# Optimization experiments

Measured on AMD Instinct MI355X. Metric: run time of the kernel, lower is better.

## Reference

```python
import jax, jax.numpy as jnp
import numpy as np

K, N, E, D = 4, 2048, 4096, 128
BETA = 0.6
EPS = 0.01           # epsilon in hard-sigmoid gating
LAM = 0.05           # lambda_schedule
TC0, TCMAX = 0.3, 0.7
COS_EPS = 1e-8       # F.cosine_similarity eps
MAX_SCORED_EDGES = 500
EDGE_DENSITY = 0.008


def setup_inputs() -> dict:
    key = jax.random.key(0)
    ks = jax.random.split(key, 8)
    s = 0.02
    H = (jax.random.uniform(ks[0], (K, N, E)) < EDGE_DENSITY).astype(jnp.float32)
    X = jax.random.normal(ks[1], (N, D), jnp.float32)
    return dict(
        H=H, X=X, epoch=50,
        mlp_w1=jax.random.normal(ks[2], (K, D, D), jnp.float32) * s,
        mlp_b1=jnp.zeros((K, D), jnp.float32),
        mlp_w2=jax.random.normal(ks[3], (K, D, D), jnp.float32) * s,
        mlp_b2=jnp.zeros((K, D), jnp.float32),
        comp_W=jax.random.normal(ks[4], (K, D, D), jnp.float32) * 0.01,
        att_w1=jax.random.normal(ks[5], (K, D, D // 2), jnp.float32) * s,
        att_b1=jnp.zeros((K, D // 2), jnp.float32),
        att_w2=jax.random.normal(ks[6], (K, D // 2, 1), jnp.float32) * s,
        att_b2=jnp.zeros((K, 1), jnp.float32),
    )


def reference(H, X, epoch, mlp_w1, mlp_b1, mlp_w2, mlp_b2, comp_W,
              att_w1, att_b1, att_w2, att_b2):
    # ---- component level (Eq. 4, batched over K) ----
    h1 = jax.nn.relu(jnp.einsum('nd,kdh->knh', X, mlp_w1) + mlp_b1[:, None, :])
    Xk = jnp.einsum('knh,khe->kne', h1, mlp_w2) + mlp_b2[:, None, :]        # [K,N,D]
    a1 = jax.nn.relu(jnp.einsum('knd,kdh->knh', Xk, att_w1) + att_b1[:, None, :])
    att = jax.nn.sigmoid(jnp.einsum('knh,kho->kno', a1, att_w2) + att_b2[:, None, :])
    S_att = att.mean(axis=(1, 2))                                            # [K]
    frob = jnp.sqrt((comp_W ** 2).sum(axis=(1, 2)))                          # ||W_k||_F
    featn = jnp.sqrt((Xk ** 2).sum(axis=(1, 2)))                             # ||MLP(X_k)||_2 (Frobenius)
    imp = BETA * frob * featn + (1.0 - BETA) * S_att
    pi_c = jax.nn.softmax(imp)
    theta_c = TC0 + (1.0 - jnp.exp(-LAM * epoch)) * (TCMAX - TC0)            # Eq. 3 schedule
    gates = jnp.clip((pi_c - theta_c) / EPS + 0.5, 0.0, 1.0)                 # hard sigmoid
    # K_min = max(1, int(0.1*K)) = 1 -> force top-1 gate open
    keep = jax.nn.one_hot(jnp.argmax(gates), K, dtype=gates.dtype)
    gates = jnp.maximum(gates, keep)

    xnorm = jnp.linalg.norm(X, axis=1)                                       # [N]
    xhat = X / jnp.maximum(xnorm, COS_EPS)[:, None]
    er = jnp.arange(E)
    eye = jnp.eye(N, dtype=bool)

    Hp_l, eg_l, npi_l = [], [], []
    for k in range(K):  # small fixed component count
        Hk = H[k]
        mask = Hk > 0                                                        # [N,E]
        cnt = mask.sum(axis=0)                                               # nodes per hyperedge
        order = jnp.cumsum(mask, axis=0)
        i = jnp.argmax(mask, axis=0)                                         # first incident node
        j = jnp.argmax(mask & (order == 2), axis=0)                          # second incident node
        cos = (xhat[i] * xhat[j]).sum(-1)                                    # [E]
        A = Hk[i, er] * Hk[j, er]                                            # A_ij per edge
        # torch loop: only first 500 edges scored; <2-node edges get 0.1; rest 0
        imp_e = jnp.where(er < MAX_SCORED_EDGES,
                          jnp.where(cnt >= 2, A * cos, 0.1), 0.0)
        pi_e = jax.nn.softmax(imp_e)
        theta_e = jnp.minimum(theta_c, pi_e.mean() + jnp.std(pi_e, ddof=1))  # torch.std unbiased
        eg = jnp.clip((pi_e - theta_e) / EPS + 0.5, 0.0, 1.0)
        eg = jnp.where((eg.sum() < 1.0) & (er == jnp.argmax(pi_e)), 1.0, eg)
        eg_eff = jnp.where(gates[k] > 0.5, eg, jnp.ones_like(eg))
        Hp = Hk * gates[k] * eg_eff[None, :]                                 # pruned incidence

        # ---- node level (Eq. 7) on pruned graph ----
        B = (Hp > 0).astype(Hk.dtype)
        Adj = ((B @ B.T) > 0) & (~eye)                                       # shared-hyperedge neighbors
        degf = Adj.sum(axis=1).astype(Hk.dtype)
        nsum = Adj.astype(Hk.dtype) @ xhat                                   # sum of neighbor unit vecs
        avg = jnp.where(degf > 0, (xhat * nsum).sum(-1) / jnp.maximum(degf, 1.0), 0.0)
        npi = jax.nn.softmax(avg * xnorm)
        Hp_l.append(Hp); eg_l.append(eg); npi_l.append(npi)

    return (jnp.stack(Hp_l), gates, jnp.stack(eg_l), jnp.stack(npi_l))
```

## Files before the change

### kernel.cpp

```cpp
#include <hip/hip_runtime.h>
#include <math.h>

#define KCOMP 4
#define NN 2048
#define EE 4096
#define DD 128
#define MAXNE 96
#define MAXSE 500
#define BETA_C 0.6f
#define EPS_G 0.01f
#define LAM_S 0.05f
#define TC0_C 0.3f
#define TCMAX_C 0.7f
#define COS_EPS_C 1e-8f

static const size_t OFF_XHAT   = 0;
static const size_t OFF_XNORM  = 1048576;
static const size_t OFF_SCAL   = 1056768;
static const size_t OFF_NCNT   = 1057024;
static const size_t OFF_EMASK  = 1089792;
static const size_t OFF_NELIST = 5284096;
static const size_t OFF_IMPE   = 6856960;
static const size_t OFF_EGS    = 6865152;
static const size_t OFF_Z      = 6930688;

__global__ __launch_bounds__(1024) void k_scanx(
    const float4* __restrict__ H4, unsigned* __restrict__ emask,
    const float* __restrict__ X, float* __restrict__ xhat, float* __restrict__ xnorm,
    float* __restrict__ scal) {
  int b = blockIdx.x, t = threadIdx.x;
  if (b < 256) {
    __shared__ unsigned lds[256 * 17];
    int k = b >> 6;
    int rem = b & 63;
    int ch_super = rem >> 4;
    int e4_super = rem & 15;
    int chi = t >> 6;
    int e4i = t & 63;
    int ch = ch_super * 16 + chi;
    int e4 = e4_super * 64 + e4i;
    int n0 = ch * 32;
    const float4* p = H4 + ((size_t)(k * NN + n0)) * (EE / 4) + e4;
    unsigned w0 = 0, w1 = 0, w2 = 0, w3 = 0;
    for (int rb = 0; rb < 32; rb += 8) {
      float4 v[8];
#pragma unroll
      for (int u = 0; u < 8; ++u) v[u] = p[(size_t)(rb + u) * (EE / 4)];
#pragma unroll
      for (int u = 0; u < 8; ++u) {
        unsigned bit = 1u << (rb + u);
        w0 |= (v[u].x > 0.f) ? bit : 0u;
        w1 |= (v[u].y > 0.f) ? bit : 0u;
        w2 |= (v[u].z > 0.f) ? bit : 0u;
        w3 |= (v[u].w > 0.f) ? bit : 0u;
      }
    }
    int el = e4i * 4;
    lds[(el + 0) * 17 + chi] = w0;
    lds[(el + 1) * 17 + chi] = w1;
    lds[(el + 2) * 17 + chi] = w2;
    lds[(el + 3) * 17 + chi] = w3;
    __syncthreads();
    int e_base = e4_super * 256;
    int wi = t & 15;
    int eo = t >> 4;
#pragma unroll
    for (int it = 0; it < 4; ++it) {
      int e_local = it * 64 + eo;
      emask[((size_t)(k * EE) + e_base + e_local) * 64 + ch_super * 16 + wi] =
          lds[e_local * 17 + wi];
    }
  } else {
    if (b == 256 && t < 64) scal[t] = 0.f;
    int node = (b - 256) * 16 + (t >> 6);
    int lane = t & 63;
    float2 v = ((const float2*)X)[(size_t)node * 64 + lane];
    float ss = v.x * v.x + v.y * v.y;
    for (int o = 32; o > 0; o >>= 1) ss += __shfl_xor(ss, o, 64);
    float nrm = sqrtf(ss);
    float den = fmaxf(nrm, COS_EPS_C);
    if (lane == 0) xnorm[node] = nrm;
    float2 o2; o2.x = v.x / den; o2.y = v.y / den;
    ((float2*)xhat)[(size_t)node * 64 + lane] = o2;
  }
}

__global__ void k_mlnel(const float* __restrict__ X,
                        const float* __restrict__ w1, const float* __restrict__ b1,
                        const float* __restrict__ w2, const float* __restrict__ b2,
                        const float* __restrict__ aw1, const float* __restrict__ ab1,
                        const float* __restrict__ aw2, const float* __restrict__ ab2,
                        const float4* __restrict__ compW4, float* __restrict__ scal,
                        const unsigned* __restrict__ emask, int* __restrict__ ncnt,
                        unsigned short* __restrict__ nelist, const float* __restrict__ xhat,
                        float* __restrict__ impE) {
  __shared__ char smem[28736];
  int t = threadIdx.x;
  int k = blockIdx.y;
  int bx = blockIdx.x;
  if (bx >= 208) {
    int e = (bx - 208) * 4 + (t >> 6);
    int lane = t & 63;
    unsigned w = emask[((size_t)(k * EE) + e) * 64 + lane];
    int pc = __popc(w);
    for (int o = 32; o > 0; o >>= 1) pc += __shfl_xor(pc, o, 64);
    float impv = 0.1f;
    if (pc >= 2) {
      unsigned l1 = w ? (unsigned)((lane << 5) + __builtin_ctz(w)) : 0xffffffffu;
      unsigned wr = w & (w - 1);
      unsigned l2 = wr ? (unsigned)((lane << 5) + __builtin_ctz(wr)) : 0xffffffffu;
      unsigned g1 = l1;
      for (int o = 32; o > 0; o >>= 1) {
        unsigned x = (unsigned)__shfl_xor((int)g1, o, 64);
        g1 = g1 < x ? g1 : x;
      }
      unsigned cand = (l1 == g1) ? l2 : l1;
      unsigned g2 = cand;
      for (int o = 32; o > 0; o >>= 1) {
        unsigned x = (unsigned)__shfl_xor((int)g2, o, 64);
        g2 = g2 < x ? g2 : x;
      }
      float2 xi = ((const float2*)xhat)[(size_t)g1 * 64 + lane];
      float2 xj = ((const float2*)xhat)[(size_t)g2 * 64 + lane];
      float d = xi.x * xj.x + xi.y * xj.y;
      for (int o = 32; o > 0; o >>= 1) d += __shfl_xor(d, o, 64);
      impv = d;
    }
    if (lane == 0) impE[k * 512 + e] = impv;
    return;
  }
  if (bx >= 144) {
    unsigned short* lst = (unsigned short*)smem;
    int* lcnt = (int*)(smem + 32 * MAXNE * 2);
    int w = bx - 144;
    if (t < 32) lcnt[t] = 0;
    __syncthreads();
    for (int e = t; e < EE; e += 256) {
      unsigned wd = emask[((size_t)(k * EE) + e) * 64 + w];
      while (wd) {
        int b = __builtin_ctz(wd); wd &= wd - 1;
        int slot = atomicAdd(&lcnt[b], 1);
        if (slot < MAXNE) lst[b * MAXNE + slot] = (unsigned short)e;
      }
    }
    __syncthreads();
    if (t < 32) ncnt[k * NN + w * 32 + t] = lcnt[t];
    for (int i = t; i < 32 * MAXNE; i += 256) {
      int b = i / MAXNE, s = i - b * MAXNE;
      int c = lcnt[b]; if (c > MAXNE) c = MAXNE;
      if (s < c) nelist[((size_t)(k * NN + w * 32 + b)) * MAXNE + s] = lst[b * MAXNE + s];
    }
    return;
  }
  float* Xs  = (float*)smem;
  float* H1s = Xs + 2048;
  float* XKs = H1s + 2048;
  float* A1s = XKs + 2048;
  float* red = A1s + 1024;
  if (bx >= 128) {
    float4 v = compW4[(size_t)k * 4096 + (bx - 128) * 256 + t];
    float s = v.x * v.x + v.y * v.y + v.z * v.z + v.w * v.w;
    for (int o = 32; o > 0; o >>= 1) s += __shfl_xor(s, o, 64);
    if ((t & 63) == 0) red[t >> 6] = s;
    __syncthreads();
    if (t == 0) atomicAdd(&scal[8 + k], red[0] + red[1] + red[2] + red[3]);
    return;
  }
  int n0 = bx * 16;
  for (int i = t; i < 16 * 128; i += 256) Xs[i] = X[(size_t)n0 * 128 + i];
  __syncthreads();

  int h = t & 127, g = t >> 7;
  const float* W1 = w1 + (size_t)k * 128 * 128;
  float acc[8];
  float bb = b1[k * 128 + h];
#pragma unroll
  for (int i = 0; i < 8; i++) acc[i] = bb;
  for (int d = 0; d < 128; ++d) {
    float w = W1[d * 128 + h];
#pragma unroll
    for (int i = 0; i < 8; i++) acc[i] = fmaf(Xs[(g * 8 + i) * 128 + d], w, acc[i]);
  }
#pragma unroll
  for (int i = 0; i < 8; i++) H1s[(g * 8 + i) * 128 + h] = fmaxf(acc[i], 0.f);
  __syncthreads();

  const float* W2 = w2 + (size_t)k * 128 * 128;
  bb = b2[k * 128 + h];
#pragma unroll
  for (int i = 0; i < 8; i++) acc[i] = bb;
  for (int d = 0; d < 128; ++d) {
    float w = W2[d * 128 + h];
#pragma unroll
    for (int i = 0; i < 8; i++) acc[i] = fmaf(H1s[(g * 8 + i) * 128 + d], w, acc[i]);
  }
  float fpart = 0.f;
#pragma unroll
  for (int i = 0; i < 8; i++) { XKs[(g * 8 + i) * 128 + h] = acc[i]; fpart = fmaf(acc[i], acc[i], fpart); }
  __syncthreads();

  int h2 = t & 63, g4 = t >> 6;
  const float* AW1 = aw1 + (size_t)k * 128 * 64;
  float a4[4];
  float ab = ab1[k * 64 + h2];
#pragma unroll
  for (int i = 0; i < 4; i++) a4[i] = ab;
  for (int d = 0; d < 128; ++d) {
    float w = AW1[d * 64 + h2];
#pragma unroll
    for (int i = 0; i < 4; i++) a4[i] = fmaf(XKs[(g4 * 4 + i) * 128 + d], w, a4[i]);
  }
#pragma unroll
  for (int i = 0; i < 4; i++) A1s[(g4 * 4 + i) * 64 + h2] = fmaxf(a4[i], 0.f);
  __syncthreads();

  float attsum = 0.f;
  if (t < 16) {
    const float* AW2 = aw2 + (size_t)k * 64;
    float a = ab2[k];
    for (int d = 0; d < 64; ++d) a = fmaf(A1s[t * 64 + d], AW2[d], a);
    attsum = 1.f / (1.f + expf(-a));
  }
  for (int o = 32; o > 0; o >>= 1) {
    fpart  += __shfl_xor(fpart, o, 64);
    attsum += __shfl_xor(attsum, o, 64);
  }
  int wv = t >> 6, ln = t & 63;
  if (ln == 0) { red[wv] = fpart; red[8 + wv] = attsum; }
  __syncthreads();
  if (t == 0) {
    float fs = red[0] + red[1] + red[2] + red[3];
    float as = red[8] + red[9] + red[10] + red[11];
    atomicAdd(&scal[0 + k], fs);
    atomicAdd(&scal[4 + k], as);
  }
}

__device__ __forceinline__ float blockReduceSum16(float v, float* red, int t) {
  for (int o = 32; o > 0; o >>= 1) v += __shfl_xor(v, o, 64);
  __syncthreads();
  if ((t & 63) == 0) red[t >> 6] = v;
  __syncthreads();
  float s = red[0];
#pragma unroll
  for (int i = 1; i < 16; i++) s += red[i];
  return s;
}

__global__ void k_edgegate(const float* __restrict__ impE, float* __restrict__ scal,
                           const int* __restrict__ epoch, float* __restrict__ out_gates,
                           float* __restrict__ egscaled, float* __restrict__ out_eg) {
  __shared__ float red[16];
  __shared__ int redi[16];
  int k = blockIdx.x;
  int t = threadIdx.x;
  float gates[KCOMP];
  float tc;
  {
    float imp[KCOMP];
    for (int kk = 0; kk < KCOMP; kk++) {
      float featn = sqrtf(scal[0 + kk]);
      float satt  = scal[4 + kk] / (float)NN;
      float frob  = sqrtf(scal[8 + kk]);
      imp[kk] = BETA_C * frob * featn + (1.f - BETA_C) * satt;
    }
    float mx = imp[0];
    for (int kk = 1; kk < KCOMP; kk++) mx = fmaxf(mx, imp[kk]);
    float ex[KCOMP], ssum = 0.f;
    for (int kk = 0; kk < KCOMP; kk++) { ex[kk] = expf(imp[kk] - mx); ssum += ex[kk]; }
    tc = TC0_C + (1.f - expf(-LAM_S * (float)epoch[0])) * (TCMAX_C - TC0_C);
    for (int kk = 0; kk < KCOMP; kk++) {
      float pi = ex[kk] / ssum;
      gates[kk] = fminf(fmaxf((pi - tc) / EPS_G + 0.5f, 0.f), 1.f);
    }
    int am = 0; float bv2 = gates[0];
    for (int kk = 1; kk < KCOMP; kk++) if (gates[kk] > bv2) { bv2 = gates[kk]; am = kk; }
    gates[am] = fmaxf(gates[am], 1.f);
  }
  if (t == 0) {
    scal[12 + k] = gates[k];
    if (k == 0) for (int kk = 0; kk < KCOMP; kk++) out_gates[kk] = gates[kk];
  }
  float imp[4];
#pragma unroll
  for (int j = 0; j < 4; j++) {
    int e = t + j * 1024;
    imp[j] = (e < MAXSE) ? impE[k * 512 + e] : 0.f;
  }
  float m = fmaxf(fmaxf(imp[0], imp[1]), fmaxf(imp[2], imp[3]));
  for (int o = 32; o > 0; o >>= 1) m = fmaxf(m, __shfl_xor(m, o, 64));
  __syncthreads();
  if ((t & 63) == 0) red[t >> 6] = m;
  __syncthreads();
  m = red[0];
#pragma unroll
  for (int i = 1; i < 16; i++) m = fmaxf(m, red[i]);
  float p[4], psum = 0.f;
#pragma unroll
  for (int j = 0; j < 4; j++) { p[j] = expf(imp[j] - m); psum += p[j]; }
  float S = blockReduceSum16(psum, red, t);
  float pi[4], tot = 0.f;
#pragma unroll
  for (int j = 0; j < 4; j++) { pi[j] = p[j] / S; tot += pi[j]; }
  float T = blockReduceSum16(tot, red, t);
  float mean = T / (float)EE;
  float devs = 0.f;
#pragma unroll
  for (int j = 0; j < 4; j++) { float d = pi[j] - mean; devs = fmaf(d, d, devs); }
  float V = blockReduceSum16(devs, red, t);
  float stdv = sqrtf(V / (float)(EE - 1));
  float theta = fminf(tc, mean + stdv);
  float eg[4], egsum = 0.f;
#pragma unroll
  for (int j = 0; j < 4; j++) {
    eg[j] = fminf(fmaxf((pi[j] - theta) / EPS_G + 0.5f, 0.f), 1.f);
    egsum += eg[j];
  }
  float EGS = blockReduceSum16(egsum, red, t);
  float bv = -1e30f; int bi = 0x7fffffff;
#pragma unroll
  for (int j = 0; j < 4; j++) if (pi[j] > bv) { bv = pi[j]; bi = t + j * 1024; }
  for (int o = 32; o > 0; o >>= 1) {
    float ov = __shfl_xor(bv, o, 64); int oi = __shfl_xor(bi, o, 64);
    if (ov > bv || (ov == bv && oi < bi)) { bv = ov; bi = oi; }
  }
  __syncthreads();
  if ((t & 63) == 0) { red[t >> 6] = bv; redi[t >> 6] = bi; }
  __syncthreads();
  float abv = red[0]; int abi = redi[0];
#pragma unroll
  for (int i = 1; i < 16; i++) {
    float ov = red[i]; int oi = redi[i];
    if (ov > abv || (ov == abv && oi < abi)) { abv = ov; abi = oi; }
  }
  float g = gates[k];
#pragma unroll
  for (int j = 0; j < 4; j++) {
    int e = t + j * 1024;
    float egv = eg[j];
    if (EGS < 1.f && e == abi) egv = 1.f;
    out_eg[(size_t)k * EE + e] = egv;
    float eff = (g > 0.5f) ? egv : 1.f;
    egscaled[k * EE + e] = g * eff;
  }
}

__global__ void k_hprow(const unsigned* __restrict__ emask,
                        const int* __restrict__ ncnt, const unsigned short* __restrict__ nelist,
                        const float* __restrict__ egs, const float* __restrict__ scal,
                        const float* __restrict__ xhat, const float* __restrict__ xnorm,
                        float* __restrict__ out, float* __restrict__ z) {
  __shared__ float row[EE];
  __shared__ unsigned short elds[MAXNE];
  __shared__ unsigned wpart[4][64];
  __shared__ unsigned short list[2048];
  __shared__ int cnt_s;
  __shared__ float sred[4];
  int k = blockIdx.y, n = blockIdx.x, t = threadIdx.x;
  float g = scal[12 + k];
  float4* o4 = (float4*)(out + ((size_t)(k * NN + n)) * EE);
  if (g <= 0.f) {
    float4 z4 = {0.f, 0.f, 0.f, 0.f};
#pragma unroll
    for (int i = 0; i < 4; i++) o4[t + i * 256] = z4;
    if (t == 0) z[k * NN + n] = 0.f;
    return;
  }
  int ec = ncnt[k * NN + n]; if (ec > MAXNE) ec = MAXNE;
  if (t < ec) elds[t] = nelist[((size_t)(k * NN + n)) * MAXNE + t];
  float4* row4 = (float4*)row;
  float4 z4 = {0.f, 0.f, 0.f, 0.f};
#pragma unroll
  for (int i = 0; i < 4; i++) row4[t + i * 256] = z4;
  if (t == 0) cnt_s = 0;
  __syncthreads();
  if (t < ec) {
    int e = elds[t];
    row[e] = egs[k * EE + e];
  }
  __syncthreads();
#pragma unroll
  for (int i = 0; i < 4; i++) o4[t + i * 256] = row4[t + i * 256];
  int lane = t & 63, wv = t >> 6;
  unsigned acc = 0;
  for (int it = wv; it < ec; it += 4) {
    int e = (int)elds[it];
    if (row[e] > 0.f) acc |= emask[((size_t)(k * EE) + e) * 64 + lane];
  }
  wpart[wv][lane] = acc;
  __syncthreads();
  if (t < 64) {
    unsigned w = wpart[0][t] | wpart[1][t] | wpart[2][t] | wpart[3][t];
    if (t == (n >> 5)) w &= ~(1u << (n & 31));
    int c = __popc(w);
    if (c > 0) {
      int base = atomicAdd(&cnt_s, c);
      while (w) {
        int b = __builtin_ctz(w); w &= w - 1;
        list[base++] = (unsigned short)((t << 5) + b);
      }
    }
  }
  __syncthreads();
  int cnt = cnt_s;
  if (cnt == 0) { if (t == 0) z[k * NN + n] = 0.f; return; }
  int fc = lane & 31, hh = lane >> 5;
  float4 xn4 = ((const float4*)xhat)[(size_t)n * 32 + fc];
  float a = 0.f;
  for (int it = wv * 2 + hh; it < cnt; it += 8) {
    int m = (int)list[it];
    float4 xm = ((const float4*)xhat)[(size_t)m * 32 + fc];
    a += xn4.x * xm.x + xn4.y * xm.y + xn4.z * xm.z + xn4.w * xm.w;
  }
  for (int o = 32; o > 0; o >>= 1) a += __shfl_xor(a, o, 64);
  if (lane == 0) sred[wv] = a;
  __syncthreads();
  if (t == 0) {
    float s = sred[0] + sred[1] + sred[2] + sred[3];
    z[k * NN + n] = (s / (float)cnt) * xnorm[n];
  }
}

__global__ void k_npi(const float* __restrict__ z, float* __restrict__ out_npi) {
  __shared__ float red[4];
  int k = blockIdx.x, t = threadIdx.x;
  float v[8]; float m = -1e30f;
#pragma unroll
  for (int j = 0; j < 8; j++) { v[j] = z[k * NN + t + j * 256]; m = fmaxf(m, v[j]); }
  for (int o = 32; o > 0; o >>= 1) m = fmaxf(m, __shfl_xor(m, o, 64));
  if ((t & 63) == 0) red[t >> 6] = m;
  __syncthreads();
  m = fmaxf(fmaxf(red[0], red[1]), fmaxf(red[2], red[3]));
  __syncthreads();
  float pe[8]; float s = 0.f;
#pragma unroll
  for (int j = 0; j < 8; j++) { pe[j] = expf(v[j] - m); s += pe[j]; }
  for (int o = 32; o > 0; o >>= 1) s += __shfl_xor(s, o, 64);
  if ((t & 63) == 0) red[t >> 6] = s;
  __syncthreads();
  s = red[0] + red[1] + red[2] + red[3];
#pragma unroll
  for (int j = 0; j < 8; j++) out_npi[k * NN + t + j * 256] = pe[j] / s;
}

extern "C" void kernel_launch(void* const* d_in, const int* in_sizes, int n_in,
                              void* d_out, int out_size, void* d_ws, size_t ws_size,
                              hipStream_t stream) {
  const float* H     = (const float*)d_in[0];
  const float* X     = (const float*)d_in[1];
  const int*   epoch = (const int*)d_in[2];
  const float* w1    = (const float*)d_in[3];
  const float* b1    = (const float*)d_in[4];
  const float* w2    = (const float*)d_in[5];
  const float* b2    = (const float*)d_in[6];
  const float* compW = (const float*)d_in[7];
  const float* aw1   = (const float*)d_in[8];
  const float* ab1   = (const float*)d_in[9];
  const float* aw2   = (const float*)d_in[10];
  const float* ab2   = (const float*)d_in[11];

  char* ws = (char*)d_ws;
  float* xhat  = (float*)(ws + OFF_XHAT);
  float* xnorm = (float*)(ws + OFF_XNORM);
  float* scal  = (float*)(ws + OFF_SCAL);
  int*   ncnt  = (int*)(ws + OFF_NCNT);
  unsigned* emask = (unsigned*)(ws + OFF_EMASK);
  unsigned short* nelist = (unsigned short*)(ws + OFF_NELIST);
  float* impE  = (float*)(ws + OFF_IMPE);
  float* egs   = (float*)(ws + OFF_EGS);
  float* zbuf  = (float*)(ws + OFF_Z);

  float* out       = (float*)d_out;
  float* out_gates = out + (size_t)KCOMP * NN * EE;
  float* out_eg    = out_gates + KCOMP;
  float* out_npi   = out_eg + (size_t)KCOMP * EE;

  k_scanx<<<384, 1024, 0, stream>>>((const float4*)H, emask, X, xhat, xnorm, scal);
  k_mlnel<<<dim3(333, KCOMP), 256, 0, stream>>>(X, w1, b1, w2, b2, aw1, ab1, aw2, ab2,
                                                (const float4*)compW, scal,
                                                emask, ncnt, nelist, xhat, impE);
  k_edgegate<<<KCOMP, 1024, 0, stream>>>(impE, scal, epoch, out_gates, egs, out_eg);
  k_hprow<<<dim3(NN, KCOMP), 256, 0, stream>>>(emask, ncnt, nelist, egs, scal, xhat, xnorm,
                                               out, zbuf);
  k_npi<<<KCOMP, 256, 0, stream>>>(zbuf, out_npi);
}
```

Baseline: 352.5 us.

## Fuse five kernels into three using last-block-done reductions

```diff
diff --git a/kernel.cpp b/kernel.cpp
--- a/kernel.cpp
+++ b/kernel.cpp
@@ -23,14 +23,24 @@
 static const size_t OFF_IMPE   = 6856960;
 static const size_t OFF_EGS    = 6865152;
 static const size_t OFF_Z      = 6930688;
-
-__global__ __launch_bounds__(1024) void k_scanx(
+static const size_t OFF_FEAT   = 6963456;
+static const size_t OFF_ATT    = 6965504;
+static const size_t OFF_FROB   = 6967552;
+
+__global__ __launch_bounds__(1024) void k_d1(
     const float4* __restrict__ H4, unsigned* __restrict__ emask,
     const float* __restrict__ X, float* __restrict__ xhat, float* __restrict__ xnorm,
-    float* __restrict__ scal) {
+    float* __restrict__ scal,
+    const float* __restrict__ w1, const float* __restrict__ b1,
+    const float* __restrict__ w2, const float* __restrict__ b2,
+    const float* __restrict__ aw1, const float* __restrict__ ab1,
+    const float* __restrict__ aw2, const float* __restrict__ ab2,
+    const float4* __restrict__ compW4,
+    float* __restrict__ featA, float* __restrict__ attA, float* __restrict__ frobA) {
+  __shared__ char smem[28928];
   int b = blockIdx.x, t = threadIdx.x;
   if (b < 256) {
-    __shared__ unsigned lds[256 * 17];
+    unsigned* lds = (unsigned*)smem;
     int k = b >> 6;
     int rem = b & 63;
     int ch_super = rem >> 4;
@@ -41,7 +51,7 @@
     int e4 = e4_super * 64 + e4i;
     int n0 = ch * 32;
     const float4* p = H4 + ((size_t)(k * NN + n0)) * (EE / 4) + e4;
-    unsigned w0 = 0, w1 = 0, w2 = 0, w3 = 0;
+    unsigned w0 = 0, w1b = 0, w2b = 0, w3 = 0;
     for (int rb = 0; rb < 32; rb += 8) {
       float4 v[8];
 #pragma unroll
@@ -49,16 +59,16 @@
 #pragma unroll
       for (int u = 0; u < 8; ++u) {
         unsigned bit = 1u << (rb + u);
-        w0 |= (v[u].x > 0.f) ? bit : 0u;
-        w1 |= (v[u].y > 0.f) ? bit : 0u;
-        w2 |= (v[u].z > 0.f) ? bit : 0u;
-        w3 |= (v[u].w > 0.f) ? bit : 0u;
+        w0  |= (v[u].x > 0.f) ? bit : 0u;
+        w1b |= (v[u].y > 0.f) ? bit : 0u;
+        w2b |= (v[u].z > 0.f) ? bit : 0u;
+        w3  |= (v[u].w > 0.f) ? bit : 0u;
       }
     }
     int el = e4i * 4;
     lds[(el + 0) * 17 + chi] = w0;
-    lds[(el + 1) * 17 + chi] = w1;
-    lds[(el + 2) * 17 + chi] = w2;
+    lds[(el + 1) * 17 + chi] = w1b;
+    lds[(el + 2) * 17 + chi] = w2b;
     lds[(el + 3) * 17 + chi] = w3;
     __syncthreads();
     int e_base = e4_super * 256;
@@ -70,7 +80,9 @@
       emask[((size_t)(k * EE) + e_base + e_local) * 64 + ch_super * 16 + wi] =
           lds[e_local * 17 + wi];
     }
-  } else {
+    return;
+  }
+  if (b < 384) {
     if (b == 256 && t < 64) scal[t] = 0.f;
     int node = (b - 256) * 16 + (t >> 6);
     int lane = t & 63;
@@ -82,24 +94,138 @@
     if (lane == 0) xnorm[node] = nrm;
     float2 o2; o2.x = v.x / den; o2.y = v.y / den;
     ((float2*)xhat)[(size_t)node * 64 + lane] = o2;
+    return;
+  }
+  if (b < 896) {
+    int mb = b - 384;
+    int k = mb >> 7;
+    int bx = mb & 127;
+    float* Xs  = (float*)smem;
+    float* H1s = Xs + 2048;
+    float* XKs = H1s + 2048;
+    float* A1s = XKs + 2048;
+    float* red = A1s + 1024;
+    int n0 = bx * 16;
+    for (int i = t; i < 16 * 128; i += 1024) Xs[i] = X[(size_t)n0 * 128 + i];
+    __syncthreads();
+
+    int h = t & 127, g = t >> 7;
+    const float* W1 = w1 + (size_t)k * 128 * 128;
+    float acc0 = b1[k * 128 + h], acc1 = acc0;
+    for (int d = 0; d < 128; ++d) {
+      float w = W1[d * 128 + h];
+      acc0 = fmaf(Xs[(g * 2 + 0) * 128 + d], w, acc0);
+      acc1 = fmaf(Xs[(g * 2 + 1) * 128 + d], w, acc1);
+    }
+    H1s[(g * 2 + 0) * 128 + h] = fmaxf(acc0, 0.f);
+    H1s[(g * 2 + 1) * 128 + h] = fmaxf(acc1, 0.f);
+    __syncthreads();
+
+    const float* W2 = w2 + (size_t)k * 128 * 128;
+    acc0 = b2[k * 128 + h]; acc1 = acc0;
+    for (int d = 0; d < 128; ++d) {
+      float w = W2[d * 128 + h];
+      acc0 = fmaf(H1s[(g * 2 + 0) * 128 + d], w, acc0);
+      acc1 = fmaf(H1s[(g * 2 + 1) * 128 + d], w, acc1);
+    }
+    float fpart = fmaf(acc1, acc1, acc0 * acc0);
+    XKs[(g * 2 + 0) * 128 + h] = acc0;
+    XKs[(g * 2 + 1) * 128 + h] = acc1;
+    __syncthreads();
+
+    int h2 = t & 63, g4 = t >> 6;
+    const float* AW1 = aw1 + (size_t)k * 128 * 64;
+    float a0 = ab1[k * 64 + h2];
+    for (int d = 0; d < 128; ++d) a0 = fmaf(XKs[g4 * 128 + d], AW1[d * 64 + h2], a0);
+    A1s[g4 * 64 + h2] = fmaxf(a0, 0.f);
+    __syncthreads();
+
+    float attsum = 0.f;
+    if (t < 16) {
+      const float* AW2 = aw2 + (size_t)k * 64;
+      float a = ab2[k];
+      for (int d = 0; d < 64; ++d) a = fmaf(A1s[t * 64 + d], AW2[d], a);
+      attsum = 1.f / (1.f + expf(-a));
+    }
+    for (int o = 32; o > 0; o >>= 1) {
+      fpart  += __shfl_xor(fpart, o, 64);
+      attsum += __shfl_xor(attsum, o, 64);
+    }
+    int wv = t >> 6, ln = t & 63;
+    if (ln == 0) { red[wv] = fpart; red[16 + wv] = attsum; }
+    __syncthreads();
+    if (t == 0) {
+      float fs = 0.f, as = 0.f;
+#pragma unroll
+      for (int i = 0; i < 16; i++) { fs += red[i]; as += red[16 + i]; }
+      featA[k * 128 + bx] = fs;
+      attA[k * 128 + bx]  = as;
+    }
+    return;
+  }
+  {
+    int fb = b - 896;
+    int k = fb >> 2, idx = fb & 3;
+    float* red = (float*)smem;
+    float4 v = compW4[(size_t)k * 4096 + idx * 1024 + t];
+    float s = v.x * v.x + v.y * v.y + v.z * v.z + v.w * v.w;
+    for (int o = 32; o > 0; o >>= 1) s += __shfl_xor(s, o, 64);
+    int wv = t >> 6, ln = t & 63;
+    if (ln == 0) red[wv] = s;
+    __syncthreads();
+    if (t == 0) {
+      float fs = 0.f;
+#pragma unroll
+      for (int i = 0; i < 16; i++) fs += red[i];
+      frobA[k * 4 + idx] = fs;
+    }
   }
 }
 
-__global__ void k_mlnel(const float* __restrict__ X,
-                        const float* __restrict__ w1, const float* __restrict__ b1,
-                        const float* __restrict__ w2, const float* __restrict__ b2,
-                        const float* __restrict__ aw1, const float* __restrict__ ab1,
-                        const float* __restrict__ aw2, const float* __restrict__ ab2,
-                        const float4* __restrict__ compW4, float* __restrict__ scal,
-                        const unsigned* __restrict__ emask, int* __restrict__ ncnt,
-                        unsigned short* __restrict__ nelist, const float* __restrict__ xhat,
-                        float* __restrict__ impE) {
-  __shared__ char smem[28736];
+__device__ __forceinline__ float bsum256(float v, volatile float* red, int t) {
+  for (int o = 32; o > 0; o >>= 1) v += __shfl_xor(v, o, 64);
+  __syncthreads();
+  if ((t & 63) == 0) red[t >> 6] = v;
+  __syncthreads();
+  return red[0] + red[1] + red[2] + red[3];
+}
+
+__global__ void k_d2(const unsigned* __restrict__ emask, int* __restrict__ ncnt,
+                     unsigned short* __restrict__ nelist, const float* __restrict__ xhat,
+                     float* __restrict__ impE, float* __restrict__ scal,
+                     const float* __restrict__ featA, const float* __restrict__ attA,
+                     const float* __restrict__ frobA, const int* __restrict__ epoch,
+                     float* __restrict__ out_gates, float* __restrict__ egs,
+                     float* __restrict__ out_eg) {
+  __shared__ char smem[32 * MAXNE * 2 + 128];
   int t = threadIdx.x;
   int k = blockIdx.y;
   int bx = blockIdx.x;
-  if (bx >= 208) {
-    int e = (bx - 208) * 4 + (t >> 6);
+  if (bx < 64) {
+    unsigned short* lst = (unsigned short*)smem;
+    int* lcnt = (int*)(smem + 32 * MAXNE * 2);
+    int w = bx;
+    if (t < 32) lcnt[t] = 0;
+    __syncthreads();
+    for (int e = t; e < EE; e += 256) {
+      unsigned wd = emask[((size_t)(k * EE) + e) * 64 + w];
+      while (wd) {
+        int b2 = __builtin_ctz(wd); wd &= wd - 1;
+        int slot = atomicAdd(&lcnt[b2], 1);
+        if (slot < MAXNE) lst[b2 * MAXNE + slot] = (unsigned short)e;
+      }
+    }
+    __syncthreads();
+    if (t < 32) ncnt[k * NN + w * 32 + t] = lcnt[t];
+    for (int i = t; i < 32 * MAXNE; i += 256) {
+      int b2 = i / MAXNE, s = i - b2 * MAXNE;
+      int c = lcnt[b2]; if (c > MAXNE) c = MAXNE;
+      if (s < c) nelist[((size_t)(k * NN + w * 32 + b2)) * MAXNE + s] = lst[b2 * MAXNE + s];
+    }
+    return;
+  }
+  {
+    int e = (bx - 64) * 4 + (t >> 6);
     int lane = t & 63;
     unsigned w = emask[((size_t)(k * EE) + e) * 64 + lane];
     int pc = __popc(w);
@@ -127,147 +253,41 @@
       impv = d;
     }
     if (lane == 0) impE[k * 512 + e] = impv;
-    return;
-  }
-  if (bx >= 144) {
-    unsigned short* lst = (unsigned short*)smem;
-    int* lcnt = (int*)(smem + 32 * MAXNE * 2);
-    int w = bx - 144;
-    if (t < 32) lcnt[t] = 0;
-    __syncthreads();
-    for (int e = t; e < EE; e += 256) {
-      unsigned wd = emask[((size_t)(k * EE) + e) * 64 + w];
-      while (wd) {
-        int b = __builtin_ctz(wd); wd &= wd - 1;
-        int slot = atomicAdd(&lcnt[b], 1);
-        if (slot < MAXNE) lst[b * MAXNE + slot] = (unsigned short)e;
-      }
-    }
-    __syncthreads();
-    if (t < 32) ncnt[k * NN + w * 32 + t] = lcnt[t];
-    for (int i = t; i < 32 * MAXNE; i += 256) {
-      int b = i / MAXNE, s = i - b * MAXNE;
-      int c = lcnt[b]; if (c > MAXNE) c = MAXNE;
-      if (s < c) nelist[((size_t)(k * NN + w * 32 + b)) * MAXNE + s] = lst[b * MAXNE + s];
-    }
-    return;
-  }
-  float* Xs  = (float*)smem;
-  float* H1s = Xs + 2048;
-  float* XKs = H1s + 2048;
-  float* A1s = XKs + 2048;
-  float* red = A1s + 1024;
-  if (bx >= 128) {
-    float4 v = compW4[(size_t)k * 4096 + (bx - 128) * 256 + t];
-    float s = v.x * v.x + v.y * v.y + v.z * v.z + v.w * v.w;
-    for (int o = 32; o > 0; o >>= 1) s += __shfl_xor(s, o, 64);
-    if ((t & 63) == 0) red[t >> 6] = s;
-    __syncthreads();
-    if (t == 0) atomicAdd(&scal[8 + k], red[0] + red[1] + red[2] + red[3]);
-    return;
-  }
-  int n0 = bx * 16;
-  for (int i = t; i < 16 * 128; i += 256) Xs[i] = X[(size_t)n0 * 128 + i];
-  __syncthreads();
-
-  int h = t & 127, g = t >> 7;
-  const float* W1 = w1 + (size_t)k * 128 * 128;
-  float acc[8];
-  float bb = b1[k * 128 + h];
-#pragma unroll
-  for (int i = 0; i < 8; i++) acc[i] = bb;
-  for (int d = 0; d < 128; ++d) {
-    float w = W1[d * 128 + h];
-#pragma unroll
-    for (int i = 0; i < 8; i++) acc[i] = fmaf(Xs[(g * 8 + i) * 128 + d], w, acc[i]);
-  }
-#pragma unroll
-  for (int i = 0; i < 8; i++) H1s[(g * 8 + i) * 128 + h] = fmaxf(acc[i], 0.f);
-  __syncthreads();
-
-  const float* W2 = w2 + (size_t)k * 128 * 128;
-  bb = b2[k * 128 + h];
-#pragma unroll
-  for (int i = 0; i < 8; i++) acc[i] = bb;
-  for (int d = 0; d < 128; ++d) {
-    float w = W2[d * 128 + h];
-#pragma unroll
-    for (int i = 0; i < 8; i++) acc[i] = fmaf(H1s[(g * 8 + i) * 128 + d], w, acc[i]);
-  }
-  float fpart = 0.f;
-#pragma unroll
-  for (int i = 0; i < 8; i++) { XKs[(g * 8 + i) * 128 + h] = acc[i]; fpart = fmaf(acc[i], acc[i], fpart); }
-  __syncthreads();
-
-  int h2 = t & 63, g4 = t >> 6;
-  const float* AW1 = aw1 + (size_t)k * 128 * 64;
-  float a4[4];
-  float ab = ab1[k * 64 + h2];
-#pragma unroll
-  for (int i = 0; i < 4; i++) a4[i] = ab;
-  for (int d = 0; d < 128; ++d) {
-    float w = AW1[d * 64 + h2];
-#pragma unroll
-    for (int i = 0; i < 4; i++) a4[i] = fmaf(XKs[(g4 * 4 + i) * 128 + d], w, a4[i]);
-  }
-#pragma unroll
-  for (int i = 0; i < 4; i++) A1s[(g4 * 4 + i) * 64 + h2] = fmaxf(a4[i], 0.f);
-  __syncthreads();
-
-  float attsum = 0.f;
-  if (t < 16) {
-    const float* AW2 = aw2 + (size_t)k * 64;
-    float a = ab2[k];
-    for (int d = 0; d < 64; ++d) a = fmaf(A1s[t * 64 + d], AW2[d], a);
-    attsum = 1.f / (1.f + expf(-a));
-  }
-  for (int o = 32; o > 0; o >>= 1) {
-    fpart  += __shfl_xor(fpart, o, 64);
-    attsum += __shfl_xor(attsum, o, 64);
-  }
+  }
+  __threadfence();
+  __shared__ int lastf;
+  if (t == 0) {
+    int old = atomicAdd((int*)scal + 16 + k, 1);
+    lastf = (old == 124);
+  }
+  __syncthreads();
+  if (!lastf) return;
+  __threadfence();
+
   int wv = t >> 6, ln = t & 63;
-  if (ln == 0) { red[wv] = fpart; red[8 + wv] = attsum; }
-  __syncthreads();
-  if (t == 0) {
-    float fs = red[0] + red[1] + red[2] + red[3];
-    float as = red[8] + red[9] + red[10] + red[11];
-    atomicAdd(&scal[0 + k], fs);
-    atomicAdd(&scal[4 + k], as);
-  }
-}
-
-__device__ __forceinline__ float blockReduceSum16(float v, float* red, int t) {
-  for (int o = 32; o > 0; o >>= 1) v += __shfl_xor(v, o, 64);
-  __syncthreads();
-  if ((t & 63) == 0) red[t >> 6] = v;
-  __syncthreads();
-  float s = red[0];
-#pragma unroll
-  for (int i = 1; i < 16; i++) s += red[i];
-  return s;
-}
-
-__global__ void k_edgegate(const float* __restrict__ impE, float* __restrict__ scal,
-                           const int* __restrict__ epoch, float* __restrict__ out_gates,
-                           float* __restrict__ egscaled, float* __restrict__ out_eg) {
-  __shared__ float red[16];
-  __shared__ int redi[16];
-  int k = blockIdx.x;
-  int t = threadIdx.x;
+  __shared__ float imps[KCOMP];
+  __shared__ float redf[4];
+  __shared__ int   redi[4];
+  {
+    float pf = 0.f, pa = 0.f;
+    for (int i = ln; i < 128; i += 64) { pf += featA[wv * 128 + i]; pa += attA[wv * 128 + i]; }
+    float pr = (ln < 4) ? frobA[wv * 4 + ln] : 0.f;
+    for (int o = 32; o > 0; o >>= 1) {
+      pf += __shfl_xor(pf, o, 64);
+      pa += __shfl_xor(pa, o, 64);
+      pr += __shfl_xor(pr, o, 64);
+    }
+    if (ln == 0)
+      imps[wv] = BETA_C * sqrtf(pr) * sqrtf(pf) + (1.f - BETA_C) * (pa / (float)NN);
+  }
+  __syncthreads();
   float gates[KCOMP];
   float tc;
   {
-    float imp[KCOMP];
-    for (int kk = 0; kk < KCOMP; kk++) {
-      float featn = sqrtf(scal[0 + kk]);
-      float satt  = scal[4 + kk] / (float)NN;
-      float frob  = sqrtf(scal[8 + kk]);
-      imp[kk] = BETA_C * frob * featn + (1.f - BETA_C) * satt;
-    }
-    float mx = imp[0];
-    for (int kk = 1; kk < KCOMP; kk++) mx = fmaxf(mx, imp[kk]);
+    float mx = imps[0];
+    for (int kk = 1; kk < KCOMP; kk++) mx = fmaxf(mx, imps[kk]);
     float ex[KCOMP], ssum = 0.f;
-    for (int kk = 0; kk < KCOMP; kk++) { ex[kk] = expf(imp[kk] - mx); ssum += ex[kk]; }
+    for (int kk = 0; kk < KCOMP; kk++) { ex[kk] = expf(imps[kk] - mx); ssum += ex[kk]; }
     tc = TC0_C + (1.f - expf(-LAM_S * (float)epoch[0])) * (TCMAX_C - TC0_C);
     for (int kk = 0; kk < KCOMP; kk++) {
       float pi = ex[kk] / ssum;
@@ -281,81 +301,88 @@
     scal[12 + k] = gates[k];
     if (k == 0) for (int kk = 0; kk < KCOMP; kk++) out_gates[kk] = gates[kk];
   }
-  float imp[4];
-#pragma unroll
-  for (int j = 0; j < 4; j++) {
-    int e = t + j * 1024;
-    imp[j] = (e < MAXSE) ? impE[k * 512 + e] : 0.f;
-  }
-  float m = fmaxf(fmaxf(imp[0], imp[1]), fmaxf(imp[2], imp[3]));
+
+  float ipj[16];
+#pragma unroll
+  for (int j = 0; j < 16; j++) {
+    int e = t + j * 256;
+    ipj[j] = (e < MAXSE) ? impE[k * 512 + e] : 0.f;
+  }
+  float m = ipj[0];
+#pragma unroll
+  for (int j = 1; j < 16; j++) m = fmaxf(m, ipj[j]);
   for (int o = 32; o > 0; o >>= 1) m = fmaxf(m, __shfl_xor(m, o, 64));
   __syncthreads();
-  if ((t & 63) == 0) red[t >> 6] = m;
-  __syncthreads();
-  m = red[0];
-#pragma unroll
-  for (int i = 1; i < 16; i++) m = fmaxf(m, red[i]);
-  float p[4], psum = 0.f;
-#pragma unroll
-  for (int j = 0; j < 4; j++) { p[j] = expf(imp[j] - m); psum += p[j]; }
-  float S = blockReduceSum16(psum, red, t);
-  float pi[4], tot = 0.f;
-#pragma unroll
-  for (int j = 0; j < 4; j++) { pi[j] = p[j] / S; tot += pi[j]; }
-  float T = blockReduceSum16(tot, red, t);
+  if (ln == 0) redf[wv] = m;
+  __syncthreads();
+  m = fmaxf(fmaxf(redf[0], redf[1]), fmaxf(redf[2], redf[3]));
+  float psum = 0.f;
+#pragma unroll
+  for (int j = 0; j < 16; j++) { ipj[j] = expf(ipj[j] - m); psum += ipj[j]; }
+  float S = bsum256(psum, redf, t);
+  float tot = 0.f;
+#pragma unroll
+  for (int j = 0; j < 16; j++) tot += ipj[j] / S;
+  float T = bsum256(tot, redf, t);
   float mean = T / (float)EE;
   float devs = 0.f;
 #pragma unroll
-  for (int j = 0; j < 4; j++) { float d = pi[j] - mean; devs = fmaf(d, d, devs); }
-  float V = blockReduceSum16(devs, red, t);
+  for (int j = 0; j < 16; j++) { float d = ipj[j] / S - mean; devs = fmaf(d, d, devs); }
+  float V = bsum256(devs, redf, t);
   float stdv = sqrtf(V / (float)(EE - 1));
   float theta = fminf(tc, mean + stdv);
-  float eg[4], egsum = 0.f;
-#pragma unroll
-  for (int j = 0; j < 4; j++) {
-    eg[j] = fminf(fmaxf((pi[j] - theta) / EPS_G + 0.5f, 0.f), 1.f);
-    egsum += eg[j];
-  }
-  float EGS = blockReduceSum16(egsum, red, t);
+  float egv[16];
+  float egsum = 0.f;
+#pragma unroll
+  for (int j = 0; j < 16; j++) {
+    egv[j] = fminf(fmaxf((ipj[j] / S - theta) / EPS_G + 0.5f, 0.f), 1.f);
+    egsum += egv[j];
+  }
+  float EGS = bsum256(egsum, redf, t);
   float bv = -1e30f; int bi = 0x7fffffff;
 #pragma unroll
-  for (int j = 0; j < 4; j++) if (pi[j] > bv) { bv = pi[j]; bi = t + j * 1024; }
+  for (int j = 0; j < 16; j++) {
+    float pi = ipj[j] / S;
+    if (pi > bv) { bv = pi; bi = t + j * 256; }
+  }
   for (int o = 32; o > 0; o >>= 1) {
     float ov = __shfl_xor(bv, o, 64); int oi = __shfl_xor(bi, o, 64);
     if (ov > bv || (ov == bv && oi < bi)) { bv = ov; bi = oi; }
   }
   __syncthreads();
-  if ((t & 63) == 0) { red[t >> 6] = bv; redi[t >> 6] = bi; }
-  __syncthreads();
-  float abv = red[0]; int abi = redi[0];
-#pragma unroll
-  for (int i = 1; i < 16; i++) {
-    float ov = red[i]; int oi = redi[i];
+  if (ln == 0) { redf[wv] = bv; redi[wv] = bi; }
+  __syncthreads();
+  float abv = redf[0]; int abi = redi[0];
+#pragma unroll
+  for (int i = 1; i < 4; i++) {
+    float ov = redf[i]; int oi = redi[i];
     if (ov > abv || (ov == abv && oi < abi)) { abv = ov; abi = oi; }
   }
   float g = gates[k];
 #pragma unroll
-  for (int j = 0; j < 4; j++) {
-    int e = t + j * 1024;
-    float egv = eg[j];
-    if (EGS < 1.f && e == abi) egv = 1.f;
-    out_eg[(size_t)k * EE + e] = egv;
-    float eff = (g > 0.5f) ? egv : 1.f;
-    egscaled[k * EE + e] = g * eff;
+  for (int j = 0; j < 16; j++) {
+    int e = t + j * 256;
+    float v = egv[j];
+    if (EGS < 1.f && e == abi) v = 1.f;
+    out_eg[(size_t)k * EE + e] = v;
+    float eff = (g > 0.5f) ? v : 1.f;
+    egs[k * EE + e] = g * eff;
   }
 }
 
 __global__ void k_hprow(const unsigned* __restrict__ emask,
                         const int* __restrict__ ncnt, const unsigned short* __restrict__ nelist,
-                        const float* __restrict__ egs, const float* __restrict__ scal,
+                        const float* __restrict__ egs, float* __restrict__ scal,
                         const float* __restrict__ xhat, const float* __restrict__ xnorm,
-                        float* __restrict__ out, float* __restrict__ z) {
+                        float* __restrict__ out, float* __restrict__ z,
+                        float* __restrict__ out_npi) {
   __shared__ float row[EE];
   __shared__ unsigned short elds[MAXNE];
   __shared__ unsigned wpart[4][64];
   __shared__ unsigned short list[2048];
   __shared__ int cnt_s;
   __shared__ float sred[4];
+  __shared__ int lastf;
   int k = blockIdx.y, n = blockIdx.x, t = threadIdx.x;
   float g = scal[12 + k];
   float4* o4 = (float4*)(out + ((size_t)(k * NN + n)) * EE);
@@ -364,83 +391,88 @@
 #pragma unroll
     for (int i = 0; i < 4; i++) o4[t + i * 256] = z4;
     if (t == 0) z[k * NN + n] = 0.f;
-    return;
-  }
-  int ec = ncnt[k * NN + n]; if (ec > MAXNE) ec = MAXNE;
-  if (t < ec) elds[t] = nelist[((size_t)(k * NN + n)) * MAXNE + t];
-  float4* row4 = (float4*)row;
-  float4 z4 = {0.f, 0.f, 0.f, 0.f};
-#pragma unroll
-  for (int i = 0; i < 4; i++) row4[t + i * 256] = z4;
-  if (t == 0) cnt_s = 0;
-  __syncthreads();
-  if (t < ec) {
-    int e = elds[t];
-    row[e] = egs[k * EE + e];
-  }
-  __syncthreads();
-#pragma unroll
-  for (int i = 0; i < 4; i++) o4[t + i * 256] = row4[t + i * 256];
-  int lane = t & 63, wv = t >> 6;
-  unsigned acc = 0;
-  for (int it = wv; it < ec; it += 4) {
-    int e = (int)elds[it];
-    if (row[e] > 0.f) acc |= emask[((size_t)(k * EE) + e) * 64 + lane];
-  }
-  wpart[wv][lane] = acc;
-  __syncthreads();
-  if (t < 64) {
-    unsigned w = wpart[0][t] | wpart[1][t] | wpart[2][t] | wpart[3][t];
-    if (t == (n >> 5)) w &= ~(1u << (n & 31));
-    int c = __popc(w);
-    if (c > 0) {
-      int base = atomicAdd(&cnt_s, c);
-      while (w) {
-        int b = __builtin_ctz(w); w &= w - 1;
-        list[base++] = (unsigned short)((t << 5) + b);
-      }
-    }
-  }
-  __syncthreads();
-  int cnt = cnt_s;
-  if (cnt == 0) { if (t == 0) z[k * NN + n] = 0.f; return; }
-  int fc = lane & 31, hh = lane >> 5;
-  float4 xn4 = ((const float4*)xhat)[(size_t)n * 32 + fc];
-  float a = 0.f;
-  for (int it = wv * 2 + hh; it < cnt; it += 8) {
-    int m = (int)list[it];
-    float4 xm = ((const float4*)xhat)[(size_t)m * 32 + fc];
-    a += xn4.x * xm.x + xn4.y * xm.y + xn4.z * xm.z + xn4.w * xm.w;
-  }
-  for (int o = 32; o > 0; o >>= 1) a += __shfl_xor(a, o, 64);
-  if (lane == 0) sred[wv] = a;
-  __syncthreads();
-  if (t == 0) {
-    float s = sred[0] + sred[1] + sred[2] + sred[3];
-    z[k * NN + n] = (s / (float)cnt) * xnorm[n];
-  }
-}
-
-__global__ void k_npi(const float* __restrict__ z, float* __restrict__ out_npi) {
-  __shared__ float red[4];
-  int k = blockIdx.x, t = threadIdx.x;
-  float v[8]; float m = -1e30f;
-#pragma unroll
-  for (int j = 0; j < 8; j++) { v[j] = z[k * NN + t + j * 256]; m = fmaxf(m, v[j]); }
-  for (int o = 32; o > 0; o >>= 1) m = fmaxf(m, __shfl_xor(m, o, 64));
-  if ((t & 63) == 0) red[t >> 6] = m;
-  __syncthreads();
-  m = fmaxf(fmaxf(red[0], red[1]), fmaxf(red[2], red[3]));
-  __syncthreads();
-  float pe[8]; float s = 0.f;
-#pragma unroll
-  for (int j = 0; j < 8; j++) { pe[j] = expf(v[j] - m); s += pe[j]; }
-  for (int o = 32; o > 0; o >>= 1) s += __shfl_xor(s, o, 64);
-  if ((t & 63) == 0) red[t >> 6] = s;
-  __syncthreads();
-  s = red[0] + red[1] + red[2] + red[3];
-#pragma unroll
-  for (int j = 0; j < 8; j++) out_npi[k * NN + t + j * 256] = pe[j] / s;
+  } else {
+    int ec = ncnt[k * NN + n]; if (ec > MAXNE) ec = MAXNE;
+    if (t < ec) elds[t] = nelist[((size_t)(k * NN + n)) * MAXNE + t];
+    float4* row4 = (float4*)row;
+    float4 z4 = {0.f, 0.f, 0.f, 0.f};
+#pragma unroll
+    for (int i = 0; i < 4; i++) row4[t + i * 256] = z4;
+    if (t == 0) cnt_s = 0;
+    __syncthreads();
+    if (t < ec) {
+      int e = elds[t];
+      row[e] = egs[k * EE + e];
+    }
+    __syncthreads();
+#pragma unroll
+    for (int i = 0; i < 4; i++) o4[t + i * 256] = row4[t + i * 256];
+    int lane = t & 63, wv = t >> 6;
+    unsigned acc = 0;
+    for (int it = wv; it < ec; it += 4) {
+      int e = (int)elds[it];
+      if (row[e] > 0.f) acc |= emask[((size_t)(k * EE) + e) * 64 + lane];
+    }
+    wpart[wv][lane] = acc;
+    __syncthreads();
+    if (t < 64) {
+      unsigned w = wpart[0][t] | wpart[1][t] | wpart[2][t] | wpart[3][t];
+      if (t == (n >> 5)) w &= ~(1u << (n & 31));
+      int c = __popc(w);
+      if (c > 0) {
+        int base = atomicAdd(&cnt_s, c);
+        while (w) {
+          int b = __builtin_ctz(w); w &= w - 1;
+          list[base++] = (unsigned short)((t << 5) + b);
+        }
+      }
+    }
+    __syncthreads();
+    int cnt = cnt_s;
+    if (cnt == 0) {
+      if (t == 0) z[k * NN + n] = 0.f;
+    } else {
+      int fc = lane & 31, hh = lane >> 5;
+      float4 xn4 = ((const float4*)xhat)[(size_t)n * 32 + fc];
+      float a = 0.f;
+      for (int it = wv * 2 + hh; it < cnt; it += 8) {
+        int m = (int)list[it];
+        float4 xm = ((const float4*)xhat)[(size_t)m * 32 + fc];
+        a += xn4.x * xm.x + xn4.y * xm.y + xn4.z * xm.z + xn4.w * xm.w;
+      }
+      for (int o = 32; o > 0; o >>= 1) a += __shfl_xor(a, o, 64);
+      if (lane == 0) sred[wv] = a;
+      __syncthreads();
+      if (t == 0) {
+        float s = sred[0] + sred[1] + sred[2] + sred[3];
+        z[k * NN + n] = (s / (float)cnt) * xnorm[n];
+      }
+    }
+  }
+  __threadfence();
+  if (t == 0) lastf = (atomicAdd((int*)scal + 20 + k, 1) == NN - 1);
+  __syncthreads();
+  if (!lastf) return;
+  __threadfence();
+  {
+    float v[8]; float m = -1e30f;
+#pragma unroll
+    for (int j = 0; j < 8; j++) { v[j] = z[k * NN + t + j * 256]; m = fmaxf(m, v[j]); }
+    for (int o = 32; o > 0; o >>= 1) m = fmaxf(m, __shfl_xor(m, o, 64));
+    if ((t & 63) == 0) sred[t >> 6] = m;
+    __syncthreads();
+    m = fmaxf(fmaxf(sred[0], sred[1]), fmaxf(sred[2], sred[3]));
+    __syncthreads();
+    float pe[8]; float s = 0.f;
+#pragma unroll
+    for (int j = 0; j < 8; j++) { pe[j] = expf(v[j] - m); s += pe[j]; }
+    for (int o = 32; o > 0; o >>= 1) s += __shfl_xor(s, o, 64);
+    if ((t & 63) == 0) sred[t >> 6] = s;
+    __syncthreads();
+    s = sred[0] + sred[1] + sred[2] + sred[3];
+#pragma unroll
+    for (int j = 0; j < 8; j++) out_npi[k * NN + t + j * 256] = pe[j] / s;
+  }
 }
 
 extern "C" void kernel_launch(void* const* d_in, const int* in_sizes, int n_in,
@@ -469,18 +501,21 @@
   float* impE  = (float*)(ws + OFF_IMPE);
   float* egs   = (float*)(ws + OFF_EGS);
   float* zbuf  = (float*)(ws + OFF_Z);
+  float* featA = (float*)(ws + OFF_FEAT);
+  float* attA  = (float*)(ws + OFF_ATT);
+  float* frobA = (float*)(ws + OFF_FROB);
 
   float* out       = (float*)d_out;
   float* out_gates = out + (size_t)KCOMP * NN * EE;
   float* out_eg    = out_gates + KCOMP;
   float* out_npi   = out_eg + (size_t)KCOMP * EE;
 
-  k_scanx<<<384, 1024, 0, stream>>>((const float4*)H, emask, X, xhat, xnorm, scal);
-  k_mlnel<<<dim3(333, KCOMP), 256, 0, stream>>>(X, w1, b1, w2, b2, aw1, ab1, aw2, ab2,
-                                                (const float4*)compW, scal,
-                                                emask, ncnt, nelist, xhat, impE);
-  k_edgegate<<<KCOMP, 1024, 0, stream>>>(impE, scal, epoch, out_gates, egs, out_eg);
+  k_d1<<<912, 1024, 0, stream>>>((const float4*)H, emask, X, xhat, xnorm, scal,
+                                 w1, b1, w2, b2, aw1, ab1, aw2, ab2,
+                                 (const float4*)compW, featA, attA, frobA);
+  k_d2<<<dim3(189, KCOMP), 256, 0, stream>>>(emask, ncnt, nelist, xhat, impE, scal,
+                                             featA, attA, frobA, epoch,
+                                             out_gates, egs, out_eg);
   k_hprow<<<dim3(NN, KCOMP), 256, 0, stream>>>(emask, ncnt, nelist, egs, scal, xhat, xnorm,
-                                               out, zbuf);
-  k_npi<<<KCOMP, 256, 0, stream>>>(zbuf, out_npi);
+                                               out, zbuf, out_npi);
 }
```

After: 1.160 ms. +229.1%, slower.
